# Performance work log

Hardware: AMD Instinct MI355X
Metric: run time of the kernel (lower is better)

## Reference

```python
import jax, jax.numpy as jnp
import numpy as np

F = 64  # filters per ConvLSTM layer

def hard_sigmoid(x):
    return jnp.clip(0.2 * x + 0.5, 0.0, 1.0)

def conv2d_same(x, w):
    # x: (B,H,W,C), w: (kh,kw,Cin,Cout)
    return jax.lax.conv_general_dilated(x, w, window_strides=(1, 1), padding='SAME',
                                        dimension_numbers=('NHWC', 'HWIO', 'NHWC'))

def convlstm2d(x_seq, Wx, Wh, b):
    # x_seq: (B,T,H,W,Cin) -> (B,T,H,W,F). Keras gate order: i, f, c, o.
    B, T, H, W, _ = x_seq.shape
    h0 = jnp.zeros((B, H, W, F), x_seq.dtype)
    c0 = h0
    def step(carry, x_t):
        h, c = carry
        z = conv2d_same(x_t, Wx) + conv2d_same(h, Wh) + b  # (B,H,W,4F)
        i, f, g, o = jnp.split(z, 4, axis=-1)
        c = hard_sigmoid(f) * c + hard_sigmoid(i) * jnp.tanh(g)
        h = hard_sigmoid(o) * jnp.tanh(c)
        return (h, c), h
    xs = jnp.moveaxis(x_seq, 1, 0)  # time-major
    _, hs = jax.lax.scan(step, (h0, c0), xs)
    return jnp.moveaxis(hs, 0, 1)

def setup_inputs() -> dict:
    key = jax.random.key(0)
    ks = jax.random.split(key, 16)
    B, n_steps, n_feat, n_out = 64, 2048, 64, 1
    s = 0.05
    def rn(k, shape):
        return jax.random.normal(k, shape, dtype=jnp.float32) * s
    inp = {'x': jax.random.normal(ks[0], (B, 1, 1, n_steps, n_feat), dtype=jnp.float32)}
    kernels = [(10, n_feat), (5, F), (10, F), (5, F)]
    for li, (kh, cin) in enumerate(kernels, start=1):
        inp[f'W{li}x'] = rn(ks[3 * li - 2], (kh, 1, cin, 4 * F))
        inp[f'W{li}h'] = rn(ks[3 * li - 1], (kh, 1, F, 4 * F))
        inp[f'b{li}'] = jnp.zeros((4 * F,), jnp.float32)
    flat_dim = 1 * 1 * n_steps * F
    inp['D1w'] = rn(ks[13], (flat_dim, 64))
    inp['D1b'] = jnp.zeros((64,), jnp.float32)
    inp['D2w'] = rn(ks[14], (64, n_out))
    inp['D2b'] = jnp.zeros((n_out,), jnp.float32)
    return inp

def reference(x, W1x, W1h, b1, W2x, W2h, b2, W3x, W3h, b3, W4x, W4h, b4, D1w, D1b, D2w, D2b):
    h = convlstm2d(x, W1x, W1h, b1)   # dropout layers are identity at inference
    h = convlstm2d(h, W2x, W2h, b2)
    h = convlstm2d(h, W3x, W3h, b3)
    h = convlstm2d(h, W4x, W4h, b4)
    flat = h.reshape(h.shape[0], -1)  # (B, T*H*W*F)
    y = jax.nn.relu(flat @ D1w + D1b)
    return y @ D2w + D2b
```

## Files before the change

kernel.cpp:

```cpp
#include <hip/hip_runtime.h>


#define TSTEPS 2048
#define TPB 4

typedef __attribute__((ext_vector_type(8))) short bf16x8;
typedef __attribute__((ext_vector_type(4))) float f32x4;

__device__ __forceinline__ unsigned short f2bf_rn(float f) {
    unsigned u = __float_as_uint(f);
    u += 0x7FFF + ((u >> 16) & 1);
    return (unsigned short)(u >> 16);
}
__device__ __forceinline__ float bf2f(unsigned short h) {
    return __uint_as_float(((unsigned)h) << 16);
}
__device__ __forceinline__ unsigned cvt_pk_bf16(float a, float b) {
    unsigned r;
    asm("v_cvt_pk_bf16_f32 %0, %1, %2" : "=v"(r) : "v"(a), "v"(b));
    return r;
}
__device__ __forceinline__ float hsig(float x) {
    return fminf(fmaxf(fmaf(x, 0.2f, 0.5f), 0.0f), 1.0f);
}
__device__ __forceinline__ float tanh_f(float x) {
    float e = __expf(2.0f * x);
    return fmaf(-2.0f, __builtin_amdgcn_rcpf(e + 1.0f), 1.0f);
}
__device__ __forceinline__ int swz(int p, int c) {
    return p * 64 + ((((c >> 3) ^ (p & 7)) << 3) | (c & 7));
}

__global__ __launch_bounds__(256) void prep_w(
    const float* __restrict__ W1, const float* __restrict__ W2,
    const float* __restrict__ W3, const float* __restrict__ W4,
    unsigned short* __restrict__ WT)
{
    const int bid = blockIdx.x;
    const int ll = bid / 3;
    const int g  = bid - ll * 3;
    const float* W = (ll == 0) ? (W1 + 4 * 16384) :
                     (ll == 1) ? (W2 + 2 * 16384) :
                     (ll == 2) ? (W3 + 4 * 16384) : (W4 + 2 * 16384);
    const int gofs = (g == 0) ? 0 : ((g == 1) ? 128 : 192);
    unsigned short* hi = WT + ll * (2 * 192 * 64) + (g * 64) * 64;
    unsigned short* lo = hi + 192 * 64;
    const int n  = threadIdx.x & 63;
    const int c0 = threadIdx.x >> 6;
    #pragma unroll
    for (int cc = 0; cc < 16; cc++) {
        int c = cc * 4 + c0;
        float w = W[c * 256 + gofs + n];
        unsigned short h = f2bf_rn(w);
        hi[n * 64 + c] = h;
        lo[n * 64 + c] = f2bf_rn(w - bf2f(h));
    }
}

__global__ __launch_bounds__(256, 2) void fused_mfma(
    const float* __restrict__ x,
    const unsigned short* __restrict__ WT,
    const float* __restrict__ B1, const float* __restrict__ B2,
    const float* __restrict__ B3, const float* __restrict__ B4,
    const float* __restrict__ D1w, float* __restrict__ part)
{
    __shared__ __align__(16) unsigned short Hhi[TPB][4096];
    __shared__ __align__(16) unsigned short Hlo[TPB][4096];

    const int tid = threadIdx.x;
    const int lane = tid & 63;
    const int w = tid >> 6;
    const int tx = lane & 15;
    const int quad = lane >> 4;
    const int n = 16 * w + tx;
    const int tt0 = blockIdx.x * TPB;

    bf16x8 Bh[2][3], Bl[2][3];
    auto loadB = [&](int l) {
        const unsigned short* wl = WT + l * (2 * 192 * 64);
        #pragma unroll
        for (int ks = 0; ks < 2; ks++)
            #pragma unroll
            for (int g = 0; g < 3; g++) {
                const unsigned short* bp = wl + (g * 64 + n) * 64 + ks * 32 + quad * 8;
                Bh[ks][g] = *(const bf16x8*)bp;
                Bl[ks][g] = *(const bf16x8*)(bp + 192 * 64);
            }
    };

    loadB(0);

    {
        #pragma unroll
        for (int k = 0; k < 16; k++) {
            int lin4 = tid + k * 256;
            int p  = lin4 >> 6;
            int q  = lin4 & 63;
            int it = q >> 4;
            int c0 = (q & 15) * 4;
            float4 v = *(const float4*)(x + (size_t)p * 131072 + (size_t)tt0 * 64 + (size_t)q * 4);
            unsigned hh01 = cvt_pk_bf16(v.x, v.y);
            unsigned hh23 = cvt_pk_bf16(v.z, v.w);
            unsigned ll01 = cvt_pk_bf16(v.x - __uint_as_float(hh01 << 16),
                                        v.y - __uint_as_float(hh01 & 0xffff0000u));
            unsigned ll23 = cvt_pk_bf16(v.z - __uint_as_float(hh23 << 16),
                                        v.w - __uint_as_float(hh23 & 0xffff0000u));
            *(uint2*)&Hhi[it][swz(p, c0)] = make_uint2(hh01, hh23);
            *(uint2*)&Hlo[it][swz(p, c0)] = make_uint2(ll01, ll23);
        }
    }
    __syncthreads();

    #pragma unroll 1
    for (int l = 0; l < 4; l++) {
        const float* Bb = (l == 0) ? B1 : (l == 1) ? B2 : (l == 2) ? B3 : B4;
        const float bi = Bb[n];
        const float bg = Bb[128 + n];
        const float bo = Bb[192 + n];

        #pragma unroll 1
        for (int it = 0; it < TPB; it++) {
            f32x4 acc[4][3];
            #pragma unroll
            for (int m = 0; m < 4; m++) {
                acc[m][0] = (f32x4){bi, bi, bi, bi};
                acc[m][1] = (f32x4){bg, bg, bg, bg};
                acc[m][2] = (f32x4){bo, bo, bo, bo};
            }

            #pragma unroll
            for (int ks = 0; ks < 2; ks++)
                #pragma unroll
                for (int m = 0; m < 4; m++) {
                    bf16x8 Ah = *(const bf16x8*)&Hhi[it][swz(m * 16 + tx, ks * 32 + quad * 8)];
                    bf16x8 Al = *(const bf16x8*)&Hlo[it][swz(m * 16 + tx, ks * 32 + quad * 8)];
                    #pragma unroll
                    for (int g = 0; g < 3; g++) {
                        acc[m][g] = __builtin_amdgcn_mfma_f32_16x16x32_bf16(Ah, Bh[ks][g], acc[m][g], 0, 0, 0);
                        acc[m][g] = __builtin_amdgcn_mfma_f32_16x16x32_bf16(Ah, Bl[ks][g], acc[m][g], 0, 0, 0);
                        acc[m][g] = __builtin_amdgcn_mfma_f32_16x16x32_bf16(Al, Bh[ks][g], acc[m][g], 0, 0, 0);
                    }
                }

            if (it == TPB - 1 && l < 3) loadB(l + 1);

            float hv[4][4];
            #pragma unroll
            for (int m = 0; m < 4; m++)
                #pragma unroll
                for (int r = 0; r < 4; r++) {
                    float cs = hsig(acc[m][0][r]) * tanh_f(acc[m][1][r]);
                    hv[m][r] = hsig(acc[m][2][r]) * tanh_f(cs);
                }

            __syncthreads();
            #pragma unroll
            for (int m = 0; m < 4; m++)
                #pragma unroll
                for (int rp = 0; rp < 2; rp++) {
                    float a = hv[m][2 * rp], b = hv[m][2 * rp + 1];
                    int p0 = m * 16 + quad * 4 + 2 * rp;
                    unsigned pk = cvt_pk_bf16(a, b);
                    Hhi[it][swz(p0, n)]     = (unsigned short)(pk & 0xffffu);
                    Hhi[it][swz(p0 + 1, n)] = (unsigned short)(pk >> 16);
                    unsigned lk = cvt_pk_bf16(a - __uint_as_float(pk << 16),
                                              b - __uint_as_float(pk & 0xffff0000u));
                    Hlo[it][swz(p0, n)]     = (unsigned short)(lk & 0xffffu);
                    Hlo[it][swz(p0 + 1, n)] = (unsigned short)(lk >> 16);
                }
        }
    }

    const float* Wd = D1w + (size_t)tt0 * 64 * 64;
    float dv[16];
    #pragma unroll
    for (int ks = 0; ks < 2; ks++)
        #pragma unroll
        for (int jj = 0; jj < 8; jj++)
            dv[ks * 8 + jj] = Wd[(ks * 32 + quad * 8 + jj) * 64 + n];
    __syncthreads();

    f32x4 accD[4];
    #pragma unroll
    for (int m = 0; m < 4; m++) accD[m] = (f32x4){0.0f, 0.0f, 0.0f, 0.0f};

    #pragma unroll
    for (int it = 0; it < TPB; it++) {
        float dn[16];
        if (it < TPB - 1) {
            #pragma unroll
            for (int ks = 0; ks < 2; ks++)
                #pragma unroll
                for (int jj = 0; jj < 8; jj++)
                    dn[ks * 8 + jj] = Wd[(it + 1) * 4096 + (ks * 32 + quad * 8 + jj) * 64 + n];
        }
        bf16x8 Dh[2], Dl[2];
        #pragma unroll
        for (int ks = 0; ks < 2; ks++) {
            union { bf16x8 v8; unsigned u[4]; } Hu, Lu;
            #pragma unroll
            for (int q2 = 0; q2 < 4; q2++) {
                float a = dv[ks * 8 + 2 * q2], b = dv[ks * 8 + 2 * q2 + 1];
                unsigned hp = cvt_pk_bf16(a, b);
                Hu.u[q2] = hp;
                Lu.u[q2] = cvt_pk_bf16(a - __uint_as_float(hp << 16),
                                       b - __uint_as_float(hp & 0xffff0000u));
            }
            Dh[ks] = Hu.v8;
            Dl[ks] = Lu.v8;
        }
        #pragma unroll
        for (int ks = 0; ks < 2; ks++)
            #pragma unroll
            for (int m = 0; m < 4; m++) {
                bf16x8 Ah = *(const bf16x8*)&Hhi[it][swz(m * 16 + tx, ks * 32 + quad * 8)];
                bf16x8 Al = *(const bf16x8*)&Hlo[it][swz(m * 16 + tx, ks * 32 + quad * 8)];
                accD[m] = __builtin_amdgcn_mfma_f32_16x16x32_bf16(Ah, Dh[ks], accD[m], 0, 0, 0);
                accD[m] = __builtin_amdgcn_mfma_f32_16x16x32_bf16(Ah, Dl[ks], accD[m], 0, 0, 0);
                accD[m] = __builtin_amdgcn_mfma_f32_16x16x32_bf16(Al, Dh[ks], accD[m], 0, 0, 0);
            }
        if (it < TPB - 1) {
            #pragma unroll
            for (int z = 0; z < 16; z++) dv[z] = dn[z];
        }
    }

    __syncthreads();
    float* LP = (float*)&Hhi[0][0];
    #pragma unroll
    for (int m = 0; m < 4; m++)
        #pragma unroll
        for (int r = 0; r < 4; r++)
            LP[(m * 16 + quad * 4 + r) * 66 + n] = accD[m][r];
    __syncthreads();
    float* dst = part + (size_t)blockIdx.x * 4096;
    #pragma unroll
    for (int k = 0; k < 8; k++) {
        int lin2 = tid + k * 256;
        int row = lin2 >> 5;
        int c0 = (lin2 & 31) * 2;
        float2 val = *(const float2*)&LP[row * 66 + c0];
        *(float2*)&dst[row * 64 + c0] = val;
    }
}

__global__ __launch_bounds__(1024) void reduce_fused(
    const float* __restrict__ part, const float* __restrict__ D1b,
    const float* __restrict__ D2w, const float* __restrict__ D2b,
    float* __restrict__ out)
{
    __shared__ float red[16][64];
    const int b = blockIdx.x;
    const int t = threadIdx.x;
    const int j = t & 63, s = t >> 6;
    float acc = 0.0f;
    #pragma unroll 4
    for (int m = 0; m < 32; m++)
        acc += part[(size_t)(s + 16 * m) * 4096 + b * 64 + j];
    red[s][j] = acc;
    __syncthreads();
    if (t < 64) {
        float v = D1b[t];
        #pragma unroll
        for (int s2 = 0; s2 < 16; s2++) v += red[s2][t];
        v = fmaxf(v, 0.0f) * D2w[t];
        #pragma unroll
        for (int off = 32; off > 0; off >>= 1)
            v += __shfl_down(v, off, 64);
        if (t == 0) out[b] = v + D2b[0];
    }
}

extern "C" void kernel_launch(void* const* d_in, const int* in_sizes, int n_in,
                              void* d_out, int out_size, void* d_ws, size_t ws_size,
                              hipStream_t stream) {
    (void)in_sizes; (void)n_in; (void)out_size; (void)ws_size;
    const float* x   = (const float*)d_in[0];
    const float* W1x = (const float*)d_in[1];
    const float* b1  = (const float*)d_in[3];
    const float* W2x = (const float*)d_in[4];
    const float* b2  = (const float*)d_in[6];
    const float* W3x = (const float*)d_in[7];
    const float* b3  = (const float*)d_in[9];
    const float* W4x = (const float*)d_in[10];
    const float* b4  = (const float*)d_in[12];
    const float* D1w = (const float*)d_in[13];
    const float* D1b = (const float*)d_in[14];
    const float* D2w = (const float*)d_in[15];
    const float* D2b = (const float*)d_in[16];
    float* out = (float*)d_out;

    const int NBLK = TSTEPS / TPB;
    float* part = (float*)d_ws;
    unsigned short* WT = (unsigned short*)(part + (size_t)NBLK * 4096);

    prep_w<<<dim3(12), dim3(256), 0, stream>>>(W1x, W2x, W3x, W4x, WT);
    fused_mfma<<<dim3(NBLK), dim3(256), 0, stream>>>(
        x, WT, b1, b2, b3, b4, D1w, part);
    reduce_fused<<<dim3(64), dim3(1024), 0, stream>>>(part, D1b, D2w, D2b, out);
}
```

Measured before the change: 175.0 us.

## Split batch rows across 8 waves and transpose weights via LDS in prep

The fused kernel now runs 512 threads per block, with each wave handling half the batch-row tiles (2 of 4 M tiles) for its 16 gate columns. This halves per-wave MFMA work and accumulator registers and doubles the number of waves available to hide latency on the serial layer chain. The weight prep kernel now transposes through shared memory so global writes are coalesced 16-byte stores instead of scattered 2-byte stores. The reduce unroll is also raised. The cost is duplicated B-fragment loads per wave and more waves contending at each barrier.

New measurement: 191.1 us. 9.2% more time.

```diff
diff --git a/kernel.cpp b/kernel.cpp
--- a/kernel.cpp
+++ b/kernel.cpp
@@ -36,6 +36,7 @@
     const float* __restrict__ W3, const float* __restrict__ W4,
     unsigned short* __restrict__ WT)
 {
+    __shared__ unsigned short Th[64][66], Tl[64][66];
     const int bid = blockIdx.x;
     const int ll = bid / 3;
     const int g  = bid - ll * 3;
@@ -46,18 +47,29 @@
     unsigned short* hi = WT + ll * (2 * 192 * 64) + (g * 64) * 64;
     unsigned short* lo = hi + 192 * 64;
     const int n  = threadIdx.x & 63;
-    const int c0 = threadIdx.x >> 6;
+    const int wv = threadIdx.x >> 6;
     #pragma unroll
     for (int cc = 0; cc < 16; cc++) {
-        int c = cc * 4 + c0;
+        int c = wv * 16 + cc;
         float w = W[c * 256 + gofs + n];
         unsigned short h = f2bf_rn(w);
-        hi[n * 64 + c] = h;
-        lo[n * 64 + c] = f2bf_rn(w - bf2f(h));
-    }
-}
-
-__global__ __launch_bounds__(256, 2) void fused_mfma(
+        Th[c][n] = h;
+        Tl[c][n] = f2bf_rn(w - bf2f(h));
+    }
+    __syncthreads();
+    const int on = threadIdx.x >> 2;
+    const int oc = (threadIdx.x & 3) * 16;
+    unsigned short bh[16], bl[16];
+    #pragma unroll
+    for (int i = 0; i < 16; i++) { bh[i] = Th[oc + i][on]; bl[i] = Tl[oc + i][on]; }
+    #pragma unroll
+    for (int q = 0; q < 2; q++) {
+        *(uint4*)(hi + on * 64 + oc + q * 8) = *(const uint4*)&bh[q * 8];
+        *(uint4*)(lo + on * 64 + oc + q * 8) = *(const uint4*)&bl[q * 8];
+    }
+}
+
+__global__ __launch_bounds__(512, 4) void fused_mfma(
     const float* __restrict__ x,
     const unsigned short* __restrict__ WT,
     const float* __restrict__ B1, const float* __restrict__ B2,
@@ -72,7 +84,9 @@
     const int w = tid >> 6;
     const int tx = lane & 15;
     const int quad = lane >> 4;
-    const int n = 16 * w + tx;
+    const int c4 = w & 3;
+    const int mh = w >> 2;
+    const int n = 16 * c4 + tx;
     const int tt0 = blockIdx.x * TPB;
 
     bf16x8 Bh[2][3], Bl[2][3];
@@ -92,8 +106,8 @@
 
     {
         #pragma unroll
-        for (int k = 0; k < 16; k++) {
-            int lin4 = tid + k * 256;
+        for (int k = 0; k < 8; k++) {
+            int lin4 = tid + k * 512;
             int p  = lin4 >> 6;
             int q  = lin4 & 63;
             int it = q >> 4;
@@ -120,46 +134,47 @@
 
         #pragma unroll 1
         for (int it = 0; it < TPB; it++) {
-            f32x4 acc[4][3];
-            #pragma unroll
-            for (int m = 0; m < 4; m++) {
-                acc[m][0] = (f32x4){bi, bi, bi, bi};
-                acc[m][1] = (f32x4){bg, bg, bg, bg};
-                acc[m][2] = (f32x4){bo, bo, bo, bo};
+            f32x4 acc[2][3];
+            #pragma unroll
+            for (int mi = 0; mi < 2; mi++) {
+                acc[mi][0] = (f32x4){bi, bi, bi, bi};
+                acc[mi][1] = (f32x4){bg, bg, bg, bg};
+                acc[mi][2] = (f32x4){bo, bo, bo, bo};
             }
 
             #pragma unroll
             for (int ks = 0; ks < 2; ks++)
                 #pragma unroll
-                for (int m = 0; m < 4; m++) {
+                for (int mi = 0; mi < 2; mi++) {
+                    int m = 2 * mh + mi;
                     bf16x8 Ah = *(const bf16x8*)&Hhi[it][swz(m * 16 + tx, ks * 32 + quad * 8)];
                     bf16x8 Al = *(const bf16x8*)&Hlo[it][swz(m * 16 + tx, ks * 32 + quad * 8)];
                     #pragma unroll
                     for (int g = 0; g < 3; g++) {
-                        acc[m][g] = __builtin_amdgcn_mfma_f32_16x16x32_bf16(Ah, Bh[ks][g], acc[m][g], 0, 0, 0);
-                        acc[m][g] = __builtin_amdgcn_mfma_f32_16x16x32_bf16(Ah, Bl[ks][g], acc[m][g], 0, 0, 0);
-                        acc[m][g] = __builtin_amdgcn_mfma_f32_16x16x32_bf16(Al, Bh[ks][g], acc[m][g], 0, 0, 0);
+                        acc[mi][g] = __builtin_amdgcn_mfma_f32_16x16x32_bf16(Ah, Bh[ks][g], acc[mi][g], 0, 0, 0);
+                        acc[mi][g] = __builtin_amdgcn_mfma_f32_16x16x32_bf16(Ah, Bl[ks][g], acc[mi][g], 0, 0, 0);
+                        acc[mi][g] = __builtin_amdgcn_mfma_f32_16x16x32_bf16(Al, Bh[ks][g], acc[mi][g], 0, 0, 0);
                     }
                 }
 
             if (it == TPB - 1 && l < 3) loadB(l + 1);
 
-            float hv[4][4];
-            #pragma unroll
-            for (int m = 0; m < 4; m++)
+            float hv[2][4];
+            #pragma unroll
+            for (int mi = 0; mi < 2; mi++)
                 #pragma unroll
                 for (int r = 0; r < 4; r++) {
-                    float cs = hsig(acc[m][0][r]) * tanh_f(acc[m][1][r]);
-                    hv[m][r] = hsig(acc[m][2][r]) * tanh_f(cs);
+                    float cs = hsig(acc[mi][0][r]) * tanh_f(acc[mi][1][r]);
+                    hv[mi][r] = hsig(acc[mi][2][r]) * tanh_f(cs);
                 }
 
             __syncthreads();
             #pragma unroll
-            for (int m = 0; m < 4; m++)
+            for (int mi = 0; mi < 2; mi++)
                 #pragma unroll
                 for (int rp = 0; rp < 2; rp++) {
-                    float a = hv[m][2 * rp], b = hv[m][2 * rp + 1];
-                    int p0 = m * 16 + quad * 4 + 2 * rp;
+                    float a = hv[mi][2 * rp], b = hv[mi][2 * rp + 1];
+                    int p0 = (2 * mh + mi) * 16 + quad * 4 + 2 * rp;
                     unsigned pk = cvt_pk_bf16(a, b);
                     Hhi[it][swz(p0, n)]     = (unsigned short)(pk & 0xffffu);
                     Hhi[it][swz(p0 + 1, n)] = (unsigned short)(pk >> 16);
@@ -180,9 +195,9 @@
             dv[ks * 8 + jj] = Wd[(ks * 32 + quad * 8 + jj) * 64 + n];
     __syncthreads();
 
-    f32x4 accD[4];
-    #pragma unroll
-    for (int m = 0; m < 4; m++) accD[m] = (f32x4){0.0f, 0.0f, 0.0f, 0.0f};
+    f32x4 accD[2];
+    #pragma unroll
+    for (int mi = 0; mi < 2; mi++) accD[mi] = (f32x4){0.0f, 0.0f, 0.0f, 0.0f};
 
     #pragma unroll
     for (int it = 0; it < TPB; it++) {
@@ -212,12 +227,13 @@
         #pragma unroll
         for (int ks = 0; ks < 2; ks++)
             #pragma unroll
-            for (int m = 0; m < 4; m++) {
+            for (int mi = 0; mi < 2; mi++) {
+                int m = 2 * mh + mi;
                 bf16x8 Ah = *(const bf16x8*)&Hhi[it][swz(m * 16 + tx, ks * 32 + quad * 8)];
                 bf16x8 Al = *(const bf16x8*)&Hlo[it][swz(m * 16 + tx, ks * 32 + quad * 8)];
-                accD[m] = __builtin_amdgcn_mfma_f32_16x16x32_bf16(Ah, Dh[ks], accD[m], 0, 0, 0);
-                accD[m] = __builtin_amdgcn_mfma_f32_16x16x32_bf16(Ah, Dl[ks], accD[m], 0, 0, 0);
-                accD[m] = __builtin_amdgcn_mfma_f32_16x16x32_bf16(Al, Dh[ks], accD[m], 0, 0, 0);
+                accD[mi] = __builtin_amdgcn_mfma_f32_16x16x32_bf16(Ah, Dh[ks], accD[mi], 0, 0, 0);
+                accD[mi] = __builtin_amdgcn_mfma_f32_16x16x32_bf16(Ah, Dl[ks], accD[mi], 0, 0, 0);
+                accD[mi] = __builtin_amdgcn_mfma_f32_16x16x32_bf16(Al, Dh[ks], accD[mi], 0, 0, 0);
             }
         if (it < TPB - 1) {
             #pragma unroll
@@ -228,15 +244,15 @@
     __syncthreads();
     float* LP = (float*)&Hhi[0][0];
     #pragma unroll
-    for (int m = 0; m < 4; m++)
+    for (int mi = 0; mi < 2; mi++)
         #pragma unroll
         for (int r = 0; r < 4; r++)
-            LP[(m * 16 + quad * 4 + r) * 66 + n] = accD[m][r];
+            LP[((2 * mh + mi) * 16 + quad * 4 + r) * 66 + n] = accD[mi][r];
     __syncthreads();
     float* dst = part + (size_t)blockIdx.x * 4096;
     #pragma unroll
-    for (int k = 0; k < 8; k++) {
-        int lin2 = tid + k * 256;
+    for (int k = 0; k < 4; k++) {
+        int lin2 = tid + k * 512;
         int row = lin2 >> 5;
         int c0 = (lin2 & 31) * 2;
         float2 val = *(const float2*)&LP[row * 66 + c0];
@@ -254,7 +270,7 @@
     const int t = threadIdx.x;
     const int j = t & 63, s = t >> 6;
     float acc = 0.0f;
-    #pragma unroll 4
+    #pragma unroll 8
     for (int m = 0; m < 32; m++)
         acc += part[(size_t)(s + 16 * m) * 4096 + b * 64 + j];
     red[s][j] = acc;
@@ -295,7 +311,7 @@
     unsigned short* WT = (unsigned short*)(part + (size_t)NBLK * 4096);
 
     prep_w<<<dim3(12), dim3(256), 0, stream>>>(W1x, W2x, W3x, W4x, WT);
-    fused_mfma<<<dim3(NBLK), dim3(256), 0, stream>>>(
+    fused_mfma<<<dim3(NBLK), dim3(512), 0, stream>>>(
         x, WT, b1, b2, b3, b4, D1w, part);
     reduce_fused<<<dim3(64), dim3(1024), 0, stream>>>(part, D1b, D2w, D2b, out);
 }
```
